# Optimization experiments

Measured on AMD Instinct MI355X. Metric: run time of the kernel, lower is better.

The kernel has to match this reference:

```python
import jax, jax.numpy as jnp
import numpy as np

# ---- static config (mirrors init_kwargs) ----
B, N, C_IN, C_OUT = 4, 8192, 128, 256
RATIO = 0.25
M = int(N * RATIO)          # sampled centers per cloud (fps ratio)
RADIUS = 0.1
MAX_NN = 64                 # max_num_neighbors
K = 16                      # num kernel points
D_MID = C_IN // 2           # pre_mlp: in_features -> in_features // 2
KP_EXTENT = RADIUS          # kernel-point influence extent (linear influence)


def setup_inputs() -> dict:
    key = jax.random.key(0)
    ks = jax.random.split(key, 10)
    x = jax.random.normal(ks[0], (B, N, C_IN), jnp.float32)
    pos = jax.random.uniform(ks[1], (B, N, 3), jnp.float32)  # unit cube
    W_pre = jax.random.normal(ks[2], (C_IN, D_MID), jnp.float32) / np.sqrt(C_IN).astype(np.float32)
    b_pre = jnp.zeros((D_MID,), jnp.float32)
    kp_pos = jax.random.normal(ks[3], (K, 3), jnp.float32) * (0.3 * RADIUS)
    kp_W = jax.random.normal(ks[4], (K, D_MID, D_MID), jnp.float32) / np.sqrt(D_MID * K).astype(np.float32)
    W_post = jax.random.normal(ks[5], (D_MID, C_OUT), jnp.float32) / np.sqrt(D_MID).astype(np.float32)
    b_post = jnp.zeros((C_OUT,), jnp.float32)
    W_sc = jax.random.normal(ks[6], (C_IN, C_OUT), jnp.float32) / np.sqrt(C_IN).astype(np.float32)
    b_sc = jnp.zeros((C_OUT,), jnp.float32)
    return dict(x=x, pos=pos, W_pre=W_pre, b_pre=b_pre, kp_pos=kp_pos, kp_W=kp_W,
                W_post=W_post, b_post=b_post, W_sc=W_sc, b_sc=b_sc)


def _fps(p):
    """Farthest point sampling on one cloud p:[N,3] -> idx:[M] (start at point 0)."""
    mind = jnp.sum((p - p[0]) ** 2, axis=-1)  # [N]
    def step(mind, _):
        i = jnp.argmax(mind).astype(jnp.int32)
        mind = jnp.minimum(mind, jnp.sum((p - p[i]) ** 2, axis=-1))
        return mind, i
    _, rest = jax.lax.scan(step, mind, None, length=M - 1)
    return jnp.concatenate([jnp.zeros((1,), jnp.int32), rest])


def reference(x, pos, W_pre, b_pre, kp_pos, kp_W, W_post, b_post, W_sc, b_sc):
    def _cloud(xb, pb):
        # xb:[N,C_IN], pb:[N,3]
        idx = _fps(pb)                                   # [M]
        centers = pb[idx]                                # [M,3]
        # radius neighbor search: nearest MAX_NN, mask to ball of RADIUS
        d2 = jnp.sum((centers[:, None, :] - pb[None, :, :]) ** 2, axis=-1)   # [M,N]
        neg_d2, nn_idx = jax.lax.top_k(-d2, MAX_NN)      # [M,MAX_NN]
        valid = (-neg_d2) <= RADIUS ** 2                 # [M,MAX_NN]
        # pre mlp then gather neighbor features (x_j)
        x_pre = xb @ W_pre + b_pre                       # [N,D_MID]
        x_j = x_pre[nn_idx]                              # [M,MAX_NN,D_MID]
        # kernel-point conv: linear influence of each kernel point
        rel = pb[nn_idx] - centers[:, None, :]           # [M,MAX_NN,3]
        dist = jnp.sqrt(jnp.sum((rel[:, :, None, :] - kp_pos[None, None, :, :]) ** 2, axis=-1) + 1e-12)  # [M,MAX_NN,K]
        infl = jnp.maximum(1.0 - dist / KP_EXTENT, 0.0) * valid[:, :, None]
        # aggregate (sum over neighbors) per kernel point, then contract with kernel weights
        s = jnp.einsum('mek,med->mkd', infl, x_j)        # [M,K,D_MID]
        feat = jnp.einsum('mkd,kdo->mo', s, kp_W)        # [M,D_MID]
        feat = feat @ W_post + b_post                    # [M,C_OUT]
        short = xb[idx] @ W_sc + b_sc                    # residual shortcut on sampled points
        return feat + short, centers

    out_feat, out_pos = jax.vmap(_cloud)(x, pos)         # [B,M,C_OUT], [B,M,3]
    return out_feat, out_pos
```

## Files before the change

### kernel.cpp

```cpp
#include <hip/hip_runtime.h>

#define B_    4
#define N_    8192
#define CIN   128
#define COUT  256
#define M_    2048
#define K_    16
#define DM    64
#define MAXNN 64
#define CAP   128
#define R2    0.01f
#define EXT   0.1f

typedef float v2f __attribute__((ext_vector_type(2)));

__device__ __forceinline__ float d2_exact(float ax, float ay, float az,
                                          float bx, float by, float bz) {
    float dx = ax - bx, dy = ay - by, dz = az - bz;
    return __fadd_rn(__fadd_rn(__fmul_rn(dx, dx), __fmul_rn(dy, dy)), __fmul_rn(dz, dz));
}

#define DPP_STEP2(CTRL)                                                                   \
    {                                                                                     \
        unsigned tlo = (unsigned)__builtin_amdgcn_update_dpp(0, (int)klo, CTRL, 0xF, 0xF, true); \
        unsigned thi = (unsigned)__builtin_amdgcn_update_dpp(0, (int)khi, CTRL, 0xF, 0xF, true); \
        unsigned long long tk = ((unsigned long long)thi << 32) | tlo;                    \
        unsigned long long ck = ((unsigned long long)khi << 32) | klo;                    \
        if (tk > ck) { klo = tlo; khi = thi; }                                            \
    }

__global__ __launch_bounds__(512, 2) void fps_pre_kernel(const float* __restrict__ pos,
                                                         int* __restrict__ idx_out,
                                                         float* __restrict__ out_pos,
                                                         const float* __restrict__ x,
                                                         const float* __restrict__ Wp,
                                                         const float* __restrict__ bvec,
                                                         float* __restrict__ xpre) {
    __shared__ union {
        unsigned long long keySlot[4];
        struct { float Ws[CIN * DM]; float xs[32][CIN]; } p;
    } sh;

    const int t = threadIdx.x;

    if (blockIdx.x >= 4) {
        const size_t rowBase = (size_t)(blockIdx.x - 4) * 32;
        for (int i = t; i < CIN * DM; i += 512) sh.p.Ws[i] = Wp[i];
        for (int i = t; i < 32 * CIN; i += 512) {
            int r = i >> 7, c = i & 127;
            sh.p.xs[r][c] = x[(rowBase + r) * CIN + c];
        }
        __syncthreads();
        const int col = t & 63, r0 = t >> 6;
        float acc[4];
        float bias = bvec[col];
#pragma unroll
        for (int rr = 0; rr < 4; rr++) acc[rr] = bias;
        for (int c = 0; c < CIN; c++) {
            float w = sh.p.Ws[c * DM + col];
#pragma unroll
            for (int rr = 0; rr < 4; rr++) acc[rr] = fmaf(sh.p.xs[r0 + 8 * rr][c], w, acc[rr]);
        }
#pragma unroll
        for (int rr = 0; rr < 4; rr++) xpre[(rowBase + r0 + 8 * rr) * DM + col] = acc[rr];
        return;
    }

    const int b = blockIdx.x;
    const float* pb = pos + (size_t)b * N_ * 3;

    v2f px[8], py[8], pz[8], mind[8];
#pragma unroll
    for (int jj = 0; jj < 8; jj++) {
        int n0 = t + (2 * jj) * 512, n1 = n0 + 512;
        px[jj] = (v2f){pb[n0 * 3 + 0], pb[n1 * 3 + 0]};
        py[jj] = (v2f){pb[n0 * 3 + 1], pb[n1 * 3 + 1]};
        pz[jj] = (v2f){pb[n0 * 3 + 2], pb[n1 * 3 + 2]};
        mind[jj] = (v2f){1e30f, 1e30f};
    }
    float cx = pb[0], cy = pb[1], cz = pb[2];
    if (t < 4) sh.keySlot[t] = 0ull;
    if (t == 0) {
        idx_out[b * M_ + 0] = 0;
        float* op = out_pos + ((size_t)(b * M_ + 0)) * 3;
        op[0] = cx; op[1] = cy; op[2] = cz;
    }
    __syncthreads();

    for (int m = 1; m < M_; m++) {
        float bv = -1.0f; int bj = 0;
        {
#pragma clang fp contract(off)
            v2f cx2 = (v2f){cx, cx}, cy2 = (v2f){cy, cy}, cz2 = (v2f){cz, cz};
#pragma unroll
            for (int jj = 0; jj < 8; jj++) {
                v2f dx = px[jj] - cx2, dy = py[jj] - cy2, dz = pz[jj] - cz2;
                v2f d = (dx * dx + dy * dy) + dz * dz;
                v2f mo = mind[jj];
                float n0 = fminf(mo.x, d.x);
                float n1 = fminf(mo.y, d.y);
                mind[jj] = (v2f){n0, n1};
                if (n0 > bv) { bv = n0; bj = 2 * jj; }
                if (n1 > bv) { bv = n1; bj = 2 * jj + 1; }
            }
        }
        const int bn = t + (bj << 9);
        unsigned klo = ~(unsigned)bn;
        unsigned khi = __float_as_uint(bv);

        DPP_STEP2(0x111)
        DPP_STEP2(0x112)
        DPP_STEP2(0x114)
        DPP_STEP2(0x118)
        DPP_STEP2(0x142)
        DPP_STEP2(0x143)

        const int buf = m & 3;
        if ((t & 63) == 63) {
            atomicMax(&sh.keySlot[buf], ((unsigned long long)khi << 32) | klo);
        }
        __syncthreads();
        const unsigned long long k0 = sh.keySlot[buf];
        if (t == 0) sh.keySlot[(m + 2) & 3] = 0ull;
        const unsigned widx = ~(unsigned)(k0 & 0xFFFFFFFFull);
        const float* cp = pb + (size_t)widx * 3;
        cx = cp[0]; cy = cp[1]; cz = cp[2];
        if (t == 0) {
            idx_out[b * M_ + m] = (int)widx;
            float* op = out_pos + ((size_t)(b * M_ + m)) * 3;
            op[0] = cx; op[1] = cy; op[2] = cz;
        }
    }
}

__global__ __launch_bounds__(256) void conv_kernel(const float* __restrict__ pos,
                                                   const float* __restrict__ x,
                                                   const float* __restrict__ xpre,
                                                   const int* __restrict__ idxs,
                                                   const float* __restrict__ kp_pos,
                                                   const float* __restrict__ kp_W,
                                                   const float* __restrict__ W_post,
                                                   const float* __restrict__ b_post,
                                                   const float* __restrict__ W_sc,
                                                   const float* __restrict__ b_sc,
                                                   float* __restrict__ out_feat) {
    const int blk = blockIdx.x;
    const int b = blk / M_;
    const int m = blk % M_;
    const int t = threadIdx.x;

    __shared__ int   nIdx[CAP];
    __shared__ float nD2[CAP];
    __shared__ int   cntS;
    __shared__ float infl[MAXNN][K_];
    __shared__ float xj[MAXNN][DM];
    __shared__ float sS[K_ * DM];
    __shared__ float featP[4][DM];
    __shared__ float xg[CIN];

    const float* pb = pos + (size_t)b * N_ * 3;
    const int ctr = idxs[b * M_ + m];
    const float cx = pb[ctr * 3 + 0], cy = pb[ctr * 3 + 1], cz = pb[ctr * 3 + 2];

    if (t == 0) cntS = 0;
    __syncthreads();

    for (int j = 0; j < N_ / 256; j++) {
        int n = j * 256 + t;
        float x0 = pb[n * 3 + 0], y0 = pb[n * 3 + 1], z0 = pb[n * 3 + 2];
        float d = d2_exact(x0, y0, z0, cx, cy, cz);
        if (d <= R2) {
            int p = atomicAdd(&cntS, 1);
            if (p < CAP) { nIdx[p] = n; nD2[p] = d; }
        }
    }
    __syncthreads();
    int cnt = cntS; if (cnt > CAP) cnt = CAP;
    if (cnt > MAXNN) {
        if (t == 0) {
            for (int s = 0; s < MAXNN; s++) {
                int best = s;
                for (int q = s + 1; q < cnt; q++) {
                    if (nD2[q] < nD2[best] || (nD2[q] == nD2[best] && nIdx[q] < nIdx[best])) best = q;
                }
                float td = nD2[best]; nD2[best] = nD2[s]; nD2[s] = td;
                int ti = nIdx[best]; nIdx[best] = nIdx[s]; nIdx[s] = ti;
            }
        }
        __syncthreads();
        cnt = MAXNN;
    }

    if (t < cnt) {
        int n = nIdx[t];
        float rx = pb[n * 3 + 0] - cx, ry = pb[n * 3 + 1] - cy, rz = pb[n * 3 + 2] - cz;
#pragma unroll
        for (int k = 0; k < K_; k++) {
            float dx = rx - kp_pos[k * 3 + 0];
            float dy = ry - kp_pos[k * 3 + 1];
            float dz = rz - kp_pos[k * 3 + 2];
            float dist = sqrtf(dx * dx + dy * dy + dz * dz + 1e-12f);
            infl[t][k] = fmaxf(1.0f - dist / EXT, 0.0f);
        }
    }
    for (int i = t; i < cnt * DM; i += 256) {
        int e = i >> 6, d = i & 63;
        xj[e][d] = xpre[((size_t)b * N_ + nIdx[e]) * DM + d];
    }
    __syncthreads();

#pragma unroll
    for (int p = 0; p < 4; p++) {
        int pair = t + p * 256;
        int k = pair >> 6, d = pair & 63;
        float acc = 0.f;
        for (int e = 0; e < cnt; e++) acc = fmaf(infl[e][k], xj[e][d], acc);
        sS[pair] = acc;
    }
    __syncthreads();

    {
        int dprime = t & 63, ks = t >> 6;
        float acc = 0.f;
        for (int k = ks * 4; k < ks * 4 + 4; k++) {
            const float* kw = kp_W + ((size_t)k * DM) * DM + dprime;
#pragma unroll
            for (int d = 0; d < DM; d++) acc = fmaf(sS[k * DM + d], kw[d * DM], acc);
        }
        featP[ks][dprime] = acc;
    }
    __syncthreads();
    if (t < DM) featP[0][t] = featP[0][t] + featP[1][t] + featP[2][t] + featP[3][t];
    if (t < CIN) xg[t] = x[((size_t)b * N_ + ctr) * CIN + t];
    __syncthreads();

    {
        const int o = t;
        float acc = b_post[o] + b_sc[o];
#pragma unroll 8
        for (int d = 0; d < DM; d++) acc = fmaf(featP[0][d], W_post[d * COUT + o], acc);
#pragma unroll 8
        for (int c = 0; c < CIN; c++) acc = fmaf(xg[c], W_sc[c * COUT + o], acc);
        out_feat[((size_t)(b * M_ + m)) * COUT + o] = acc;
    }
}

extern "C" void kernel_launch(void* const* d_in, const int* in_sizes, int n_in,
                              void* d_out, int out_size, void* d_ws, size_t ws_size,
                              hipStream_t stream) {
    const float* x      = (const float*)d_in[0];
    const float* pos    = (const float*)d_in[1];
    const float* W_pre  = (const float*)d_in[2];
    const float* b_pre  = (const float*)d_in[3];
    const float* kp_pos = (const float*)d_in[4];
    const float* kp_W   = (const float*)d_in[5];
    const float* W_post = (const float*)d_in[6];
    const float* b_post = (const float*)d_in[7];
    const float* W_sc   = (const float*)d_in[8];
    const float* b_sc   = (const float*)d_in[9];

    float* out_feat = (float*)d_out;
    float* out_pos  = (float*)d_out + (size_t)B_ * M_ * COUT;

    int*   idxs = (int*)d_ws;
    float* xpre = (float*)((char*)d_ws + 64 * 1024);

    fps_pre_kernel<<<4 + (B_ * N_) / 32, 512, 0, stream>>>(pos, idxs, out_pos,
                                                           x, W_pre, b_pre, xpre);
    conv_kernel<<<B_ * M_, 256, 0, stream>>>(pos, x, xpre, idxs, kp_pos, kp_W,
                                             W_post, b_post, W_sc, b_sc, out_feat);
}
```

Before: 2.275 ms.

## Split FPS argmax into value max then index/coord atomicMin pass

Each FPS step now finds the block-wide maximum distance value with a float-only DPP reduction and one LDS atomicMax. It then takes a second barrier in which lanes holding that maximum publish packed index and coordinate keys via atomicMin. This lets the next center come from shared memory rather than a dependent global load of pos, and uses inline packed-FP32 asm for the distance update. The cost is a second __syncthreads per iteration and extra 64-bit LDS atomics. Launch bounds also drop the minimum of two blocks per CU.

New measurement: 2.995 ms. +31.7%, slower.

```diff
diff --git a/kernel.cpp b/kernel.cpp
--- a/kernel.cpp
+++ b/kernel.cpp
@@ -20,24 +20,40 @@
     return __fadd_rn(__fadd_rn(__fmul_rn(dx, dx), __fmul_rn(dy, dy)), __fmul_rn(dz, dz));
 }
 
-#define DPP_STEP2(CTRL)                                                                   \
-    {                                                                                     \
-        unsigned tlo = (unsigned)__builtin_amdgcn_update_dpp(0, (int)klo, CTRL, 0xF, 0xF, true); \
-        unsigned thi = (unsigned)__builtin_amdgcn_update_dpp(0, (int)khi, CTRL, 0xF, 0xF, true); \
-        unsigned long long tk = ((unsigned long long)thi << 32) | tlo;                    \
-        unsigned long long ck = ((unsigned long long)khi << 32) | klo;                    \
-        if (tk > ck) { klo = tlo; khi = thi; }                                            \
-    }
-
-__global__ __launch_bounds__(512, 2) void fps_pre_kernel(const float* __restrict__ pos,
-                                                         int* __restrict__ idx_out,
-                                                         float* __restrict__ out_pos,
-                                                         const float* __restrict__ x,
-                                                         const float* __restrict__ Wp,
-                                                         const float* __restrict__ bvec,
-                                                         float* __restrict__ xpre) {
+#define PAIR_UPD(JJ)                                                         \
+    { v2f d2v, t0v, t1v;                                                     \
+      asm("v_pk_add_f32 %0, %3, %6\n\t"                                      \
+          "v_pk_add_f32 %1, %4, %7\n\t"                                      \
+          "v_pk_add_f32 %2, %5, %8\n\t"                                      \
+          "v_pk_mul_f32 %0, %0, %0\n\t"                                      \
+          "v_pk_mul_f32 %1, %1, %1\n\t"                                      \
+          "v_pk_mul_f32 %2, %2, %2\n\t"                                      \
+          "v_pk_add_f32 %0, %0, %1\n\t"                                      \
+          "v_pk_add_f32 %0, %0, %2"                                          \
+          : "=&v"(d2v), "=&v"(t0v), "=&v"(t1v)                               \
+          : "v"(px[JJ]), "v"(py[JJ]), "v"(pz[JJ]),                           \
+            "v"(ncx2), "v"(ncy2), "v"(ncz2));                                \
+      mnd[2*(JJ)]   = fminf(mnd[2*(JJ)],   d2v.x);                           \
+      mnd[2*(JJ)+1] = fminf(mnd[2*(JJ)+1], d2v.y);                           \
+      bv0 = fmaxf(bv0, mnd[2*(JJ)]);                                         \
+      bv1 = fmaxf(bv1, mnd[2*(JJ)+1]); }
+
+#define VMAX_DPP(CTRL)                                                        \
+    red = fmaxf(red, __uint_as_float((unsigned)__builtin_amdgcn_update_dpp(   \
+                  0, (int)__float_as_uint(red), CTRL, 0xF, 0xF, true)));
+
+__global__ __launch_bounds__(512) void fps_pre_kernel(const float* __restrict__ pos,
+                                                      int* __restrict__ idx_out,
+                                                      float* __restrict__ out_pos,
+                                                      const float* __restrict__ x,
+                                                      const float* __restrict__ Wp,
+                                                      const float* __restrict__ bvec,
+                                                      float* __restrict__ xpre) {
     __shared__ union {
-        unsigned long long keySlot[4];
+        struct {
+            unsigned slotV[2];
+            unsigned long long slotC[2][3];
+        } f;
         struct { float Ws[CIN * DM]; float xs[32][CIN]; } p;
     } sh;
 
@@ -69,18 +85,23 @@
     const int b = blockIdx.x;
     const float* pb = pos + (size_t)b * N_ * 3;
 
-    v2f px[8], py[8], pz[8], mind[8];
+    v2f px[8], py[8], pz[8];
+    float mnd[16];
 #pragma unroll
     for (int jj = 0; jj < 8; jj++) {
         int n0 = t + (2 * jj) * 512, n1 = n0 + 512;
         px[jj] = (v2f){pb[n0 * 3 + 0], pb[n1 * 3 + 0]};
         py[jj] = (v2f){pb[n0 * 3 + 1], pb[n1 * 3 + 1]};
         pz[jj] = (v2f){pb[n0 * 3 + 2], pb[n1 * 3 + 2]};
-        mind[jj] = (v2f){1e30f, 1e30f};
+        mnd[2 * jj] = 1e30f; mnd[2 * jj + 1] = 1e30f;
     }
     float cx = pb[0], cy = pb[1], cz = pb[2];
-    if (t < 4) sh.keySlot[t] = 0ull;
     if (t == 0) {
+        sh.f.slotV[0] = 0u; sh.f.slotV[1] = 0u;
+#pragma unroll
+        for (int q = 0; q < 3; q++) {
+            sh.f.slotC[0][q] = ~0ull; sh.f.slotC[1][q] = ~0ull;
+        }
         idx_out[b * M_ + 0] = 0;
         float* op = out_pos + ((size_t)(b * M_ + 0)) * 3;
         op[0] = cx; op[1] = cy; op[2] = cz;
@@ -88,43 +109,62 @@
     __syncthreads();
 
     for (int m = 1; m < M_; m++) {
-        float bv = -1.0f; int bj = 0;
-        {
-#pragma clang fp contract(off)
-            v2f cx2 = (v2f){cx, cx}, cy2 = (v2f){cy, cy}, cz2 = (v2f){cz, cz};
+        const float ncx = -cx, ncy = -cy, ncz = -cz;
+        const v2f ncx2 = (v2f){ncx, ncx}, ncy2 = (v2f){ncy, ncy}, ncz2 = (v2f){ncz, ncz};
+        float bv0 = -1.0f, bv1 = -1.0f;
+        PAIR_UPD(0) PAIR_UPD(1) PAIR_UPD(2) PAIR_UPD(3)
+        PAIR_UPD(4) PAIR_UPD(5) PAIR_UPD(6) PAIR_UPD(7)
+        const float lanemax = fmaxf(bv0, bv1);
+
+        float red = lanemax;
+        VMAX_DPP(0x111)
+        VMAX_DPP(0x112)
+        VMAX_DPP(0x114)
+        VMAX_DPP(0x118)
+        VMAX_DPP(0x142)
+        VMAX_DPP(0x143)
+
+        const int buf = m & 1;
+        if ((t & 63) == 63) {
+            atomicMax(&sh.f.slotV[buf], __float_as_uint(red));
+        }
+        __syncthreads();
+
+        const unsigned gmb = sh.f.slotV[buf];
+        if (t == 0) {
+            sh.f.slotV[buf ^ 1] = 0u;
+            sh.f.slotC[buf ^ 1][0] = ~0ull;
+            sh.f.slotC[buf ^ 1][1] = ~0ull;
+            sh.f.slotC[buf ^ 1][2] = ~0ull;
+        }
+        const float gmaxf = __uint_as_float(gmb);
+        if (lanemax == gmaxf) {
+            unsigned nb = 0xFFFFFFFFu;
+            float fx = 0.f, fy = 0.f, fz = 0.f;
 #pragma unroll
             for (int jj = 0; jj < 8; jj++) {
-                v2f dx = px[jj] - cx2, dy = py[jj] - cy2, dz = pz[jj] - cz2;
-                v2f d = (dx * dx + dy * dy) + dz * dz;
-                v2f mo = mind[jj];
-                float n0 = fminf(mo.x, d.x);
-                float n1 = fminf(mo.y, d.y);
-                mind[jj] = (v2f){n0, n1};
-                if (n0 > bv) { bv = n0; bj = 2 * jj; }
-                if (n1 > bv) { bv = n1; bj = 2 * jj + 1; }
+                if (mnd[2 * jj] == gmaxf && nb == 0xFFFFFFFFu) {
+                    nb = (unsigned)(t + (2 * jj) * 512);
+                    fx = px[jj].x; fy = py[jj].x; fz = pz[jj].x;
+                }
+                if (mnd[2 * jj + 1] == gmaxf && nb == 0xFFFFFFFFu) {
+                    nb = (unsigned)(t + (2 * jj + 1) * 512);
+                    fx = px[jj].y; fy = py[jj].y; fz = pz[jj].y;
+                }
             }
-        }
-        const int bn = t + (bj << 9);
-        unsigned klo = ~(unsigned)bn;
-        unsigned khi = __float_as_uint(bv);
-
-        DPP_STEP2(0x111)
-        DPP_STEP2(0x112)
-        DPP_STEP2(0x114)
-        DPP_STEP2(0x118)
-        DPP_STEP2(0x142)
-        DPP_STEP2(0x143)
-
-        const int buf = m & 3;
-        if ((t & 63) == 63) {
-            atomicMax(&sh.keySlot[buf], ((unsigned long long)khi << 32) | klo);
+            atomicMin(&sh.f.slotC[buf][0], ((unsigned long long)nb << 32) | (unsigned long long)__float_as_uint(fx));
+            atomicMin(&sh.f.slotC[buf][1], ((unsigned long long)nb << 32) | (unsigned long long)__float_as_uint(fy));
+            atomicMin(&sh.f.slotC[buf][2], ((unsigned long long)nb << 32) | (unsigned long long)__float_as_uint(fz));
         }
         __syncthreads();
-        const unsigned long long k0 = sh.keySlot[buf];
-        if (t == 0) sh.keySlot[(m + 2) & 3] = 0ull;
-        const unsigned widx = ~(unsigned)(k0 & 0xFFFFFFFFull);
-        const float* cp = pb + (size_t)widx * 3;
-        cx = cp[0]; cy = cp[1]; cz = cp[2];
+
+        const unsigned long long kx = sh.f.slotC[buf][0];
+        const unsigned long long ky = sh.f.slotC[buf][1];
+        const unsigned long long kz = sh.f.slotC[buf][2];
+        const unsigned widx = (unsigned)(kx >> 32);
+        cx = __uint_as_float((unsigned)kx);
+        cy = __uint_as_float((unsigned)ky);
+        cz = __uint_as_float((unsigned)kz);
         if (t == 0) {
             idx_out[b * M_ + m] = (int)widx;
             float* op = out_pos + ((size_t)(b * M_ + m)) * 3;
```
